# Kernel tuning notes

Measured on AMD Instinct MI355X. Metric: run time of the kernel, lower is better.

Reference implementation:

```python
import jax, jax.numpy as jnp
import numpy as np

B, L, D, H = 2, 2048, 1024, 16
HD = D // H

def setup_inputs() -> dict:
    key = jax.random.key(0)
    ks = jax.random.split(key, 9)
    s = 1.0 / np.sqrt(D)
    return {
        "query": jax.random.normal(ks[0], (B, L, D), dtype=jnp.float32),
        "Wq": jax.random.uniform(ks[1], (D, D), jnp.float32, -s, s),
        "bq": jax.random.uniform(ks[2], (D,), jnp.float32, -s, s),
        "Wk": jax.random.uniform(ks[3], (D, D), jnp.float32, -s, s),
        "bk": jax.random.uniform(ks[4], (D,), jnp.float32, -s, s),
        "Wv": jax.random.uniform(ks[5], (D, D), jnp.float32, -s, s),
        "bv": jax.random.uniform(ks[6], (D,), jnp.float32, -s, s),
        "Wo": jax.random.uniform(ks[7], (D, D), jnp.float32, -s, s),
        "bo": jax.random.uniform(ks[8], (D,), jnp.float32, -s, s),
    }

def reference(query, Wq, bq, Wk, bk, Wv, bv, Wo, bo):
    # self-attention: key_value = query. Linear: x @ W.T + b (torch convention)
    scale = HD ** -0.5
    q = (query @ Wq.T + bq).reshape(B, L, H, HD).transpose(0, 2, 1, 3)  # (B,H,L,hd)
    k = (query @ Wk.T + bk).reshape(B, L, H, HD).transpose(0, 2, 1, 3)
    v = (query @ Wv.T + bv).reshape(B, L, H, HD).transpose(0, 2, 1, 3)
    logits = jnp.einsum('bhqd,bhkd->bhqk', q, k) * scale  # (B,H,Lq,Lk)
    attn = jax.nn.softmax(logits, axis=-1)
    out = jnp.einsum('bhqk,bhkd->bhqd', attn, v)
    out = out.transpose(0, 2, 1, 3).reshape(B, L, D)
    return out @ Wo.T + bo
```

## Files before the change

### kernel.cpp

```cpp
#include <hip/hip_runtime.h>

#define Bc 2
#define Lc 2048
#define Dc 1024
#define Hc 16
#define HDc 64
#define LOG2E 1.44269504088896340736f

typedef __bf16 bf16x8 __attribute__((ext_vector_type(8)));
typedef __bf16 bf16x2 __attribute__((ext_vector_type(2)));
typedef float f32x4 __attribute__((ext_vector_type(4)));
typedef unsigned short u16;
typedef unsigned int u32;
typedef unsigned long long u64;

__device__ __forceinline__ u16 f2bf(float x) {
    union { float f; u32 u; } c; c.f = x;
    u32 u = c.u + 0x7fffu + ((c.u >> 16) & 1u);
    return (u16)(u >> 16);
}

__device__ __forceinline__ u32 pkbf(float a, float b) {
#if __has_builtin(__builtin_amdgcn_cvt_pk_bf16_f32)
    union { bf16x2 v; u32 u; } c;
    c.v = __builtin_amdgcn_cvt_pk_bf16_f32(a, b);
    return c.u;
#else
    return (u32)f2bf(a) | ((u32)f2bf(b) << 16);
#endif
}

__device__ __forceinline__ void g2l16(const void* g, void* l) {
    __builtin_amdgcn_global_load_lds(
        (const __attribute__((address_space(1))) void*)g,
        (__attribute__((address_space(3))) void*)l, 16, 0, 0);
}

__global__ __launch_bounds__(256) void cast_bf16(
    const float* __restrict__ x,
    const float* __restrict__ wq, const float* __restrict__ wk,
    const float* __restrict__ wv, const float* __restrict__ wo,
    u16* __restrict__ xb, u16* __restrict__ wqb, u16* __restrict__ wkb,
    u16* __restrict__ wvb, u16* __restrict__ wob)
{
    const int i = blockIdx.x * 256 + threadIdx.x;
    const float* s; u16* d; int off;
    if (i < 1048576) { s = x; d = xb; off = i; }
    else {
        const int j = i - 1048576;
        const int sel = j >> 18;
        off = j & 262143;
        s = sel == 0 ? wq : sel == 1 ? wk : sel == 2 ? wv : wo;
        d = sel == 0 ? wqb : sel == 1 ? wkb : sel == 2 ? wvb : wob;
    }
    const float4 f = ((const float4*)s)[off];
    ushort4 o;
    o.x = f2bf(f.x); o.y = f2bf(f.y); o.z = f2bf(f.z); o.w = f2bf(f.w);
    ((ushort4*)d)[off] = o;
}

__device__ __forceinline__ void gemm128_body(
    const u16* __restrict__ A, const u16* __restrict__ Bm,
    int row0, int col0, int K,
    f32x4 (&acc)[4][4], u16* As, u16* Bs)
{
    const int tid  = threadIdx.x;
    const int w    = tid >> 6;
    const int lane = tid & 63;
    const int l15  = lane & 15, quad = lane >> 4;
    const int srow = lane >> 2;
    const int scol = (lane & 3) << 3;
    const int wm   = (w & 1) << 6, wn = (w >> 1) << 6;

    for (int k0 = 0; k0 < K; k0 += 32) {
        __syncthreads();
#pragma unroll
        for (int s = 0; s < 2; ++s) {
            const int r = w * 32 + s * 16;
            g2l16(&A [(size_t)(row0 + r + srow) * K + k0 + scol], &As[r * 32]);
            g2l16(&Bm[(size_t)(col0 + r + srow) * K + k0 + scol], &Bs[r * 32]);
        }
        __syncthreads();

        bf16x8 af[4], bf[4];
#pragma unroll
        for (int i = 0; i < 4; ++i)
            af[i] = *(const bf16x8*)&As[(wm + i * 16 + l15) * 32 + quad * 8];
#pragma unroll
        for (int j = 0; j < 4; ++j)
            bf[j] = *(const bf16x8*)&Bs[(wn + j * 16 + l15) * 32 + quad * 8];
#pragma unroll
        for (int i = 0; i < 4; ++i)
#pragma unroll
            for (int j = 0; j < 4; ++j)
                acc[i][j] = __builtin_amdgcn_mfma_f32_16x16x32_bf16(
                    af[i], bf[j], acc[i][j], 0, 0, 0);
    }
}

__global__ __launch_bounds__(256) void gemm_qkv_bf16(
    const u16* __restrict__ Xb,
    const u16* __restrict__ Wqb, const u16* __restrict__ Wkb, const u16* __restrict__ Wvb,
    const float* __restrict__ bq, const float* __restrict__ bk, const float* __restrict__ bv,
    u16* __restrict__ qo, u16* __restrict__ ko, u16* __restrict__ vto)
{
    __shared__ __attribute__((aligned(16))) u16 As[128 * 32];
    __shared__ __attribute__((aligned(16))) u16 Bs[128 * 32];

    const int z = blockIdx.z;
    const int tid = threadIdx.x;
    const int w = tid >> 6, lane = tid & 63;
    const int l15 = lane & 15, quad = lane >> 4;
    const int wm = (w & 1) << 6, wn = (w >> 1) << 6;

    f32x4 acc[4][4];
#pragma unroll
    for (int i = 0; i < 4; ++i)
#pragma unroll
        for (int j = 0; j < 4; ++j)
#pragma unroll
            for (int r = 0; r < 4; ++r) acc[i][j][r] = 0.0f;

    if (z == 2) {
        const int row0 = blockIdx.y << 7;
        const int col0 = blockIdx.x << 7;
        gemm128_body(Wvb, Xb, row0, col0, Dc, acc, As, Bs);

        float bvv[4][4];
#pragma unroll
        for (int i = 0; i < 4; ++i)
#pragma unroll
            for (int r = 0; r < 4; ++r)
                bvv[i][r] = bv[row0 + wm + i * 16 + quad * 4 + r];
#pragma unroll
        for (int j = 0; j < 4; ++j) {
            const int mcol = col0 + wn + j * 16 + l15;
            const int bb = mcol >> 11, ll = mcol & (Lc - 1);
#pragma unroll
            for (int i = 0; i < 4; ++i)
#pragma unroll
                for (int r = 0; r < 4; ++r) {
                    const int nrow = row0 + wm + i * 16 + quad * 4 + r;
                    const int hh = nrow >> 6, hd = nrow & 63;
                    vto[(((size_t)(bb * Hc + hh) * HDc + hd) << 11) + ll] =
                        f2bf(acc[i][j][r] + bvv[i][r]);
                }
        }
        return;
    }

    const u16*   W    = z == 0 ? Wqb : Wkb;
    const float* bias = z == 0 ? bq  : bk;
    const int row0 = blockIdx.x << 7;
    const int col0 = blockIdx.y << 7;
    gemm128_body(Xb, W, row0, col0, Dc, acc, As, Bs);

    const float qs = 0.125f * LOG2E;
#pragma unroll
    for (int j = 0; j < 4; ++j) {
        const int n  = col0 + wn + j * 16 + l15;
        const float bj = bias[n];
        const int hh = n >> 6, hd = n & 63;
#pragma unroll
        for (int i = 0; i < 4; ++i)
#pragma unroll
            for (int r = 0; r < 4; ++r) {
                const int m  = row0 + wm + i * 16 + quad * 4 + r;
                const int bb = m >> 11, ll = m & (Lc - 1);
                const float val = acc[i][j][r] + bj;
                const size_t idx = (((size_t)(bb * Hc + hh) * Lc + ll) << 6) + hd;
                if (z == 0) qo[idx] = f2bf(val * qs);
                else        ko[idx] = f2bf(val);
            }
    }
}

__global__ __launch_bounds__(256) void attn_mfma(
    const u16* __restrict__ q, const u16* __restrict__ k,
    const u16* __restrict__ vt, u16* __restrict__ out)
{
    __shared__ __attribute__((aligned(16))) u16 Ks[2][64 * 32];
    __shared__ __attribute__((aligned(16))) u16 Vs[2][64 * 32];

    const int tid = threadIdx.x;
    const int w = tid >> 6, lane = tid & 63;
    const int l15 = lane & 15, quad = lane >> 4;
    const int bh = blockIdx.x & 31;
    const int qt = blockIdx.x >> 5;
    const int h  = bh & (Hc - 1);
    const int b  = bh >> 4;
    const int l0 = qt << 7;

    const size_t bhs = (size_t)(b * Hc + h) * (Lc * HDc);
    const u16* qb = q  + bhs;
    const u16* kb = k  + bhs;
    const u16* vb = vt + bhs;

    bf16x8 qf[2][2];
#pragma unroll
    for (int mt = 0; mt < 2; ++mt) {
        const size_t row = (size_t)(l0 + w * 32 + mt * 16 + l15) * HDc;
        qf[mt][0] = *(const bf16x8*)&qb[row + quad * 8];
        qf[mt][1] = *(const bf16x8*)&qb[row + 32 + quad * 8];
    }

    const int srow  = lane >> 2;
    const int sunit = lane & 3;
    const int gd = (l15 >> 1) & 3;

    f32x4 oacc[2][4];
    float l_i[2] = {0.0f, 0.0f};
#pragma unroll
    for (int mt = 0; mt < 2; ++mt)
#pragma unroll
        for (int dt = 0; dt < 4; ++dt)
#pragma unroll
            for (int r = 0; r < 4; ++r) oacc[mt][dt][r] = 0.0f;

    for (int kt = 0; kt < Lc; kt += 64) {
        __syncthreads();
#pragma unroll
        for (int i = 0; i < 4; ++i) {
            const int c = w * 4 + i;
            const int p = (c >> 2) & 1, g = c & 3;
            const int row = g * 16 + srow;
            if (c < 8)
                g2l16(&kb[(size_t)(kt + row) * HDc + p * 32 +
                          ((sunit ^ ((row >> 1) & 3)) << 3)],
                      &Ks[p][g * 512]);
            else
                g2l16(&vb[(size_t)row * Lc + kt + p * 32 +
                          ((sunit ^ ((row >> 1) & 3)) << 3)],
                      &Vs[p][g * 512]);
        }
        __syncthreads();

        f32x4 st[2][4];
#pragma unroll
        for (int t = 0; t < 4; ++t) {
            const int j   = t * 16 + l15;
            const int off = j * 32 + ((quad ^ gd) << 3);
            const bf16x8 kf0 = *(const bf16x8*)&Ks[0][off];
            const bf16x8 kf1 = *(const bf16x8*)&Ks[1][off];
#pragma unroll
            for (int mt = 0; mt < 2; ++mt) {
                f32x4 z = {0.0f, 0.0f, 0.0f, 0.0f};
                z = __builtin_amdgcn_mfma_f32_16x16x32_bf16(kf0, qf[mt][0], z, 0, 0, 0);
                st[mt][t] = __builtin_amdgcn_mfma_f32_16x16x32_bf16(kf1, qf[mt][1], z, 0, 0, 0);
            }
        }

        u32 pk[2][4][2];
#pragma unroll
        for (int mt = 0; mt < 2; ++mt) {
            f32x4 s4 = {0.0f, 0.0f, 0.0f, 0.0f};
#pragma unroll
            for (int t = 0; t < 4; ++t) {
                f32x4 p;
#pragma unroll
                for (int r = 0; r < 4; ++r) p[r] = exp2f(st[mt][t][r]);
                s4 += p;
                pk[mt][t][0] = pkbf(p[0], p[1]);
                pk[mt][t][1] = pkbf(p[2], p[3]);
            }
            l_i[mt] += s4[0] + s4[1] + s4[2] + s4[3];
        }

#pragma unroll
        for (int cp = 0; cp < 2; ++cp) {
            union { bf16x8 v; u32 uw[4]; } pf0, pf1;
            pf0.uw[0] = pk[0][2 * cp][0];     pf0.uw[1] = pk[0][2 * cp][1];
            pf0.uw[2] = pk[0][2 * cp + 1][0]; pf0.uw[3] = pk[0][2 * cp + 1][1];
            pf1.uw[0] = pk[1][2 * cp][0];     pf1.uw[1] = pk[1][2 * cp][1];
            pf1.uw[2] = pk[1][2 * cp + 1][0]; pf1.uw[3] = pk[1][2 * cp + 1][1];
#pragma unroll
            for (int dt = 0; dt < 4; ++dt) {
                const int base = (dt * 16 + l15) * 32 + ((quad & 1) << 2);
                union { bf16x8 v; u64 d[2]; } vf;
                vf.d[0] = *(const u64*)&Vs[cp][base + (((quad >> 1) ^ gd) << 3)];
                vf.d[1] = *(const u64*)&Vs[cp][base + (((2 + (quad >> 1)) ^ gd) << 3)];
                oacc[0][dt] = __builtin_amdgcn_mfma_f32_16x16x32_bf16(
                    vf.v, pf0.v, oacc[0][dt], 0, 0, 0);
                oacc[1][dt] = __builtin_amdgcn_mfma_f32_16x16x32_bf16(
                    vf.v, pf1.v, oacc[1][dt], 0, 0, 0);
            }
        }
    }

#pragma unroll
    for (int mt = 0; mt < 2; ++mt) {
        float l = l_i[mt];
        l += __shfl_xor(l, 16);
        l += __shfl_xor(l, 32);
        const float inv = 1.0f / l;
        const int lrow = l0 + w * 32 + mt * 16 + l15;
        u16* ob = out + ((size_t)(b * Lc + lrow)) * Dc + h * HDc;
#pragma unroll
        for (int dt = 0; dt < 4; ++dt) {
            uint2 pr;
            pr.x = pkbf(oacc[mt][dt][0] * inv, oacc[mt][dt][1] * inv);
            pr.y = pkbf(oacc[mt][dt][2] * inv, oacc[mt][dt][3] * inv);
            *(uint2*)&ob[dt * 16 + quad * 4] = pr;
        }
    }
}

__global__ __launch_bounds__(256) void gemm_o_bf16(
    const u16* __restrict__ Ab, const u16* __restrict__ Wob,
    const float* __restrict__ bo, float* __restrict__ out)
{
    __shared__ __attribute__((aligned(16))) u16 As[128 * 32];
    __shared__ __attribute__((aligned(16))) u16 Bs[128 * 32];
    const int row0 = blockIdx.x << 7;
    const int col0 = blockIdx.y << 7;

    f32x4 acc[4][4];
#pragma unroll
    for (int i = 0; i < 4; ++i)
#pragma unroll
        for (int j = 0; j < 4; ++j)
#pragma unroll
            for (int r = 0; r < 4; ++r) acc[i][j][r] = 0.0f;

    gemm128_body(Ab, Wob, row0, col0, Dc, acc, As, Bs);

    const int tid = threadIdx.x;
    const int w = tid >> 6, lane = tid & 63;
    const int l15 = lane & 15, quad = lane >> 4;
    const int wm = (w & 1) << 6, wn = (w >> 1) << 6;

#pragma unroll
    for (int j = 0; j < 4; ++j) {
        const int n = col0 + wn + j * 16 + l15;
        const float bj = bo[n];
#pragma unroll
        for (int i = 0; i < 4; ++i)
#pragma unroll
            for (int r = 0; r < 4; ++r) {
                const int m = row0 + wm + i * 16 + quad * 4 + r;
                out[(size_t)m * Dc + n] = acc[i][j][r] + bj;
            }
    }
}

extern "C" void kernel_launch(void* const* d_in, const int* in_sizes, int n_in,
                              void* d_out, int out_size, void* d_ws, size_t ws_size,
                              hipStream_t stream)
{
    const float* query = (const float*)d_in[0];
    const float* Wq = (const float*)d_in[1];
    const float* bq = (const float*)d_in[2];
    const float* Wk = (const float*)d_in[3];
    const float* bk = (const float*)d_in[4];
    const float* Wv = (const float*)d_in[5];
    const float* bv = (const float*)d_in[6];
    const float* Wo = (const float*)d_in[7];
    const float* bo = (const float*)d_in[8];

    u16* ws = (u16*)d_ws;
    const size_t nX = (size_t)Bc * Lc * Dc;
    const size_t nW = (size_t)Dc * Dc;
    u16* xb  = ws;
    u16* wqb = xb + nX;
    u16* wkb = wqb + nW;
    u16* wvb = wkb + nW;
    u16* wob = wvb + nW;
    u16* q_w = wob + nW;
    u16* k_w = q_w + nX;
    u16* vt_w = k_w + nX;
    u16* a_w = vt_w + nX;

    cast_bf16<<<dim3(8192), 256, 0, stream>>>(query, Wq, Wk, Wv, Wo,
                                              xb, wqb, wkb, wvb, wob);
    gemm_qkv_bf16<<<dim3(32, 8, 3), 256, 0, stream>>>(xb, wqb, wkb, wvb,
                                                      bq, bk, bv, q_w, k_w, vt_w);
    attn_mfma<<<dim3(512), 256, 0, stream>>>(q_w, k_w, vt_w, a_w);
    gemm_o_bf16<<<dim3(32, 8), 256, 0, stream>>>(a_w, wob, bo, (float*)d_out);
}
```

Measured before the change: 228.2 us.

## Swizzle LDS with 64-wide K tiles and transpose GEMM roles for vector stores

The shared GEMM body now stages 64-wide K slices per barrier pair instead of 32. It uses an XOR-swizzled LDS layout so the per-row fragment reads avoid bank conflicts. The QKV and output projections swap operand roles, so each lane's four accumulator values are contiguous along the feature or sequence dimension. That lets the epilogues write packed bf16 uint2 or float4 vectors and load biases as float4, instead of issuing scalar scattered stores. The cost is double the LDS per block, which may reduce occupancy, plus an odd comma-operator index expression in the Q/K store.

```diff
diff --git a/kernel.cpp b/kernel.cpp
--- a/kernel.cpp
+++ b/kernel.cpp
@@ -68,33 +68,39 @@
     const int w    = tid >> 6;
     const int lane = tid & 63;
     const int l15  = lane & 15, quad = lane >> 4;
-    const int srow = lane >> 2;
-    const int scol = (lane & 3) << 3;
+    const int srow = lane >> 3;
+    const int sxor = ((lane & 7) ^ srow) << 3;
     const int wm   = (w & 1) << 6, wn = (w >> 1) << 6;
-
-    for (int k0 = 0; k0 < K; k0 += 32) {
+    const int l7   = l15 & 7;
+
+    for (int k0 = 0; k0 < K; k0 += 64) {
         __syncthreads();
 #pragma unroll
-        for (int s = 0; s < 2; ++s) {
-            const int r = w * 32 + s * 16;
-            g2l16(&A [(size_t)(row0 + r + srow) * K + k0 + scol], &As[r * 32]);
-            g2l16(&Bm[(size_t)(col0 + r + srow) * K + k0 + scol], &Bs[r * 32]);
+        for (int s = 0; s < 4; ++s) {
+            const int rb = w * 32 + s * 8;
+            g2l16(&A [(size_t)(row0 + rb + srow) * K + k0 + sxor], &As[rb * 64]);
+            g2l16(&Bm[(size_t)(col0 + rb + srow) * K + k0 + sxor], &Bs[rb * 64]);
         }
         __syncthreads();
 
-        bf16x8 af[4], bf[4];
-#pragma unroll
-        for (int i = 0; i < 4; ++i)
-            af[i] = *(const bf16x8*)&As[(wm + i * 16 + l15) * 32 + quad * 8];
-#pragma unroll
-        for (int j = 0; j < 4; ++j)
-            bf[j] = *(const bf16x8*)&Bs[(wn + j * 16 + l15) * 32 + quad * 8];
-#pragma unroll
-        for (int i = 0; i < 4; ++i)
+#pragma unroll
+        for (int kk = 0; kk < 2; ++kk) {
+            bf16x8 af[4], bf[4];
+#pragma unroll
+            for (int i = 0; i < 4; ++i)
+                af[i] = *(const bf16x8*)&As[(wm + i * 16 + l15) * 64 +
+                                            (((kk * 4 + quad) ^ l7) << 3)];
 #pragma unroll
             for (int j = 0; j < 4; ++j)
-                acc[i][j] = __builtin_amdgcn_mfma_f32_16x16x32_bf16(
-                    af[i], bf[j], acc[i][j], 0, 0, 0);
+                bf[j] = *(const bf16x8*)&Bs[(wn + j * 16 + l15) * 64 +
+                                            (((kk * 4 + quad) ^ l7) << 3)];
+#pragma unroll
+            for (int i = 0; i < 4; ++i)
+#pragma unroll
+                for (int j = 0; j < 4; ++j)
+                    acc[i][j] = __builtin_amdgcn_mfma_f32_16x16x32_bf16(
+                        af[i], bf[j], acc[i][j], 0, 0, 0);
+        }
     }
 }
 
@@ -104,8 +110,8 @@
     const float* __restrict__ bq, const float* __restrict__ bk, const float* __restrict__ bv,
     u16* __restrict__ qo, u16* __restrict__ ko, u16* __restrict__ vto)
 {
-    __shared__ __attribute__((aligned(16))) u16 As[128 * 32];
-    __shared__ __attribute__((aligned(16))) u16 Bs[128 * 32];
+    __shared__ __attribute__((aligned(16))) u16 As[128 * 64];
+    __shared__ __attribute__((aligned(16))) u16 Bs[128 * 64];
 
     const int z = blockIdx.z;
     const int tid = threadIdx.x;
@@ -122,56 +128,55 @@
             for (int r = 0; r < 4; ++r) acc[i][j][r] = 0.0f;
 
     if (z == 2) {
-        const int row0 = blockIdx.y << 7;
-        const int col0 = blockIdx.x << 7;
-        gemm128_body(Wvb, Xb, row0, col0, Dc, acc, As, Bs);
-
-        float bvv[4][4];
-#pragma unroll
-        for (int i = 0; i < 4; ++i)
-#pragma unroll
-            for (int r = 0; r < 4; ++r)
-                bvv[i][r] = bv[row0 + wm + i * 16 + quad * 4 + r];
+        const int row0 = blockIdx.x << 7;
+        const int col0 = blockIdx.y << 7;
+        gemm128_body(Xb, Wvb, row0, col0, Dc, acc, As, Bs);
+
+        const int b = row0 >> 11;
 #pragma unroll
         for (int j = 0; j < 4; ++j) {
-            const int mcol = col0 + wn + j * 16 + l15;
-            const int bb = mcol >> 11, ll = mcol & (Lc - 1);
-#pragma unroll
-            for (int i = 0; i < 4; ++i)
-#pragma unroll
-                for (int r = 0; r < 4; ++r) {
-                    const int nrow = row0 + wm + i * 16 + quad * 4 + r;
-                    const int hh = nrow >> 6, hd = nrow & 63;
-                    vto[(((size_t)(bb * Hc + hh) * HDc + hd) << 11) + ll] =
-                        f2bf(acc[i][j][r] + bvv[i][r]);
-                }
+            const int n = col0 + wn + j * 16 + l15;
+            const float bj = bv[n];
+            const int hh = n >> 6, hd = n & 63;
+            u16* vbase = vto + (((size_t)(b * Hc + hh) * HDc + hd) << 11);
+#pragma unroll
+            for (int i = 0; i < 4; ++i) {
+                const int l = (row0 + wm + i * 16 + quad * 4) & (Lc - 1);
+                uint2 pr;
+                pr.x = pkbf(acc[i][j][0] + bj, acc[i][j][1] + bj);
+                pr.y = pkbf(acc[i][j][2] + bj, acc[i][j][3] + bj);
+                *(uint2*)&vbase[l] = pr;
+            }
         }
         return;
     }
 
     const u16*   W    = z == 0 ? Wqb : Wkb;
     const float* bias = z == 0 ? bq  : bk;
-    const int row0 = blockIdx.x << 7;
-    const int col0 = blockIdx.y << 7;
-    gemm128_body(Xb, W, row0, col0, Dc, acc, As, Bs);
-
-    const float qs = 0.125f * LOG2E;
+    u16*         outp = z == 0 ? qo  : ko;
+    const int row0 = blockIdx.y << 7;
+    const int col0 = blockIdx.x << 7;
+    gemm128_body(W, Xb, row0, col0, Dc, acc, As, Bs);
+
+    const float qs = z == 0 ? 0.125f * LOG2E : 1.0f;
+    const int h = (row0 + wm) >> 6;
+    float4 b4[4];
+#pragma unroll
+    for (int i = 0; i < 4; ++i)
+        b4[i] = *(const float4*)&bias[row0 + wm + i * 16 + quad * 4];
+
 #pragma unroll
     for (int j = 0; j < 4; ++j) {
-        const int n  = col0 + wn + j * 16 + l15;
-        const float bj = bias[n];
-        const int hh = n >> 6, hd = n & 63;
-#pragma unroll
-        for (int i = 0; i < 4; ++i)
-#pragma unroll
-            for (int r = 0; r < 4; ++r) {
-                const int m  = row0 + wm + i * 16 + quad * 4 + r;
-                const int bb = m >> 11, ll = m & (Lc - 1);
-                const float val = acc[i][j][r] + bj;
-                const size_t idx = (((size_t)(bb * Hc + hh) * Lc + ll) << 6) + hd;
-                if (z == 0) qo[idx] = f2bf(val * qs);
-                else        ko[idx] = f2bf(val);
-            }
+        const int tok = col0 + wn + j * 16 + l15;
+        const int bb = tok >> 11, ll = tok & (Lc - 1);
+        u16* obase = outp + (((size_t)(bb * Hc + h) * Lc + ll) << 6);
+#pragma unroll
+        for (int i = 0; i < 4; ++i) {
+            uint2 pr;
+            pr.x = pkbf((acc[i][j][0] + b4[i].x) * qs, (acc[i][j][1] + b4[i].y) * qs);
+            pr.y = pkbf((acc[i][j][2] + b4[i].z) * qs, (acc[i][j][3] + b4[i].w) * qs);
+            *(uint2*)&obase[wm ? 0 : 0, i * 16 + quad * 4] = pr;
+        }
     }
 }
 
@@ -309,10 +314,10 @@
     const u16* __restrict__ Ab, const u16* __restrict__ Wob,
     const float* __restrict__ bo, float* __restrict__ out)
 {
-    __shared__ __attribute__((aligned(16))) u16 As[128 * 32];
-    __shared__ __attribute__((aligned(16))) u16 Bs[128 * 32];
-    const int row0 = blockIdx.x << 7;
-    const int col0 = blockIdx.y << 7;
+    __shared__ __attribute__((aligned(16))) u16 As[128 * 64];
+    __shared__ __attribute__((aligned(16))) u16 Bs[128 * 64];
+    const int row0 = blockIdx.y << 7;
+    const int col0 = blockIdx.x << 7;
 
     f32x4 acc[4][4];
 #pragma unroll
@@ -322,24 +327,29 @@
 #pragma unroll
             for (int r = 0; r < 4; ++r) acc[i][j][r] = 0.0f;
 
-    gemm128_body(Ab, Wob, row0, col0, Dc, acc, As, Bs);
+    gemm128_body(Wob, Ab, row0, col0, Dc, acc, As, Bs);
 
     const int tid = threadIdx.x;
     const int w = tid >> 6, lane = tid & 63;
     const int l15 = lane & 15, quad = lane >> 4;
     const int wm = (w & 1) << 6, wn = (w >> 1) << 6;
 
+    float4 b4[4];
+#pragma unroll
+    for (int i = 0; i < 4; ++i)
+        b4[i] = *(const float4*)&bo[row0 + wm + i * 16 + quad * 4];
+
 #pragma unroll
     for (int j = 0; j < 4; ++j) {
-        const int n = col0 + wn + j * 16 + l15;
-        const float bj = bo[n];
-#pragma unroll
-        for (int i = 0; i < 4; ++i)
-#pragma unroll
-            for (int r = 0; r < 4; ++r) {
-                const int m = row0 + wm + i * 16 + quad * 4 + r;
-                out[(size_t)m * Dc + n] = acc[i][j][r] + bj;
-            }
+        const int tok = col0 + wn + j * 16 + l15;
+        float* obase = out + (size_t)tok * Dc + row0 + wm;
+#pragma unroll
+        for (int i = 0; i < 4; ++i) {
+            float4 o;
+            o.x = acc[i][j][0] + b4[i].x; o.y = acc[i][j][1] + b4[i].y;
+            o.z = acc[i][j][2] + b4[i].z; o.w = acc[i][j][3] + b4[i].w;
+            *(float4*)&obase[i * 16 + quad * 4] = o;
+        }
     }
 }
 
```

New measurement: 226.4 us. No clear change (-0.8%).
